# Kernel optimization log

Hardware: AMD Instinct MI355X
Metric: run time of the kernel (lower is better)

The kernel has to match this reference:

```python
import jax, jax.numpy as jnp
import numpy as np

B, H, W, D = 8, 56, 56, 256
NH = 8
KD = D // NH  # 32, key_dim == head_dim (value_factor=1)
FFN = 1024
EPS = 1e-6
SCALE = KD ** -0.5


def _lin(x, w, b):
    # torch nn.Linear: y = x @ W^T + b, W is (out, in)
    return jnp.einsum('...i,oi->...o', x, w) + b


def _ln(x, g, b):
    mu = jnp.mean(x, axis=-1, keepdims=True)
    var = jnp.mean(jnp.square(x - mu), axis=-1, keepdims=True)
    return (x - mu) * jax.lax.rsqrt(var + EPS) * g + b


def _dwconv(x, kernel, bias):
    # x: (B,H,W,C) NHWC, kernel: (kh,kw,1,C) HWIO depthwise
    y = jax.lax.conv_general_dilated(
        x, kernel, window_strides=(1, 1), padding='SAME',
        dimension_numbers=('NHWC', 'HWIO', 'NHWC'),
        feature_group_count=x.shape[-1])
    return y + bias


def _rope_sincos(h, w, head_dim):
    # PosEncodingGen: angle freq repeated pairwise, index over flattened H*W
    angle = 1.0 / (10000.0 ** jnp.linspace(0.0, 1.0, head_dim // 2))
    angle = jnp.repeat(angle, 2)  # (head_dim,)
    idx = jnp.arange(h * w, dtype=jnp.float32)
    phase = idx[:, None] * angle[None, :]
    return jnp.sin(phase).reshape(h, w, head_dim), jnp.cos(phase).reshape(h, w, head_dim)


def _angle_transform(x, sin, cos):
    # x: (B,NH,H,W,KD); sin/cos: (H,W,KD) broadcast over (B,NH)
    x1 = x[..., ::2]
    x2 = x[..., 1::2]
    rot = jnp.stack([-x2, x1], axis=-1).reshape(x.shape)
    return x * cos + rot * sin


def setup_inputs() -> dict:
    key = jax.random.key(0)
    ks = jax.random.split(key, 16)
    s = 0.02
    return {
        'x': jax.random.normal(ks[0], (B, H, W, D), jnp.float32),
        'cpe_w': jax.random.normal(ks[1], (3, 3, 1, D), jnp.float32) * s,
        'cpe_b': jnp.zeros((D,), jnp.float32),
        'ln1_g': jnp.ones((D,), jnp.float32),
        'ln1_b': jnp.zeros((D,), jnp.float32),
        'wq': jax.random.normal(ks[2], (D, D), jnp.float32) * s,
        'bq': jnp.zeros((D,), jnp.float32),
        'wk': jax.random.normal(ks[3], (D, D), jnp.float32) * s,
        'bk': jnp.zeros((D,), jnp.float32),
        'wv': jax.random.normal(ks[4], (D, D), jnp.float32) * s,
        'bv': jnp.zeros((D,), jnp.float32),
        'lepe_w': jax.random.normal(ks[5], (5, 5, 1, D), jnp.float32) * s,
        'lepe_b': jnp.zeros((D,), jnp.float32),
        'wo': jax.random.normal(ks[6], (D, D), jnp.float32) * s,
        'bo': jnp.zeros((D,), jnp.float32),
        'ln2_g': jnp.ones((D,), jnp.float32),
        'ln2_b': jnp.zeros((D,), jnp.float32),
        'fc1_w': jax.random.normal(ks[7], (FFN, D), jnp.float32) * s,
        'fc1_b': jnp.zeros((FFN,), jnp.float32),
        'dw_w': jax.random.normal(ks[8], (3, 3, 1, FFN), jnp.float32) * s,
        'dw_b': jnp.zeros((FFN,), jnp.float32),
        'fc2_w': jax.random.normal(ks[9], (D, FFN), jnp.float32) * s,
        'fc2_b': jnp.zeros((D,), jnp.float32),
    }


def _decomposed_gsa(x, sin, cos, wq, bq, wk, bk, wv, bv, lepe_w, lepe_b, wo, bo):
    b, h, w, d = x.shape
    q = _lin(x, wq, bq)
    k = _lin(x, wk, bk) * SCALE
    v = _lin(x, wv, bv)
    lepe = _dwconv(v, lepe_w, lepe_b)  # (b,h,w,d)
    # -> (b, nh, h, w, kd)
    q = q.reshape(b, h, w, NH, KD).transpose(0, 3, 1, 2, 4)
    k = k.reshape(b, h, w, NH, KD).transpose(0, 3, 1, 2, 4)
    v = v.reshape(b, h, w, NH, KD).transpose(0, 3, 1, 2, 4)
    qr = _angle_transform(q, sin, cos)
    kr = _angle_transform(k, sin, cos)
    # attention along W axis (per row h)
    aw = jnp.einsum('bnhik,bnhjk->bnhij', qr, kr)  # (b,nh,h,w,w)
    aw = jax.nn.softmax(aw, axis=-1)
    vw = jnp.einsum('bnhij,bnhjd->bnhid', aw, v)   # (b,nh,h,w,kd)
    # attention along H axis (per column w)
    ah = jnp.einsum('bniwk,bnjwk->bnwij', qr, kr)  # (b,nh,w,h,h)
    ah = jax.nn.softmax(ah, axis=-1)
    out = jnp.einsum('bnwij,bnjwd->bniwd', ah, vw)  # (b,nh,h,w,kd)
    # faithful to torch: flat reinterpret of (b,nh,h,w,kd) -> (b,h,w,nh*kd)
    out = out.reshape(b, h, w, NH * KD)
    out = out + lepe
    return _lin(out, wo, bo)


def reference(x, cpe_w, cpe_b, ln1_g, ln1_b, wq, bq, wk, bk, wv, bv,
              lepe_w, lepe_b, wo, bo, ln2_g, ln2_b,
              fc1_w, fc1_b, dw_w, dw_b, fc2_w, fc2_b):
    b, h, w, d = x.shape
    x = x + _dwconv(x, cpe_w, cpe_b)
    sin, cos = _rope_sincos(h, w, KD)
    # attention sub-block
    shortcut = x
    xn = _ln(x, ln1_g, ln1_b)
    attn = _decomposed_gsa(xn, sin, cos, wq, bq, wk, bk, wv, bv,
                           lepe_w, lepe_b, wo, bo)
    x = shortcut + attn  # drop_path=Identity, gamma_1=1.0
    # FFN sub-block (subconv=True, subln=False)
    shortcut = x
    xn = _ln(x, ln2_g, ln2_b)
    hdn = jax.nn.gelu(_lin(xn, fc1_w, fc1_b), approximate=False)
    hdn = _dwconv(hdn, dw_w, dw_b) + hdn
    ffn_out = _lin(hdn, fc2_w, fc2_b)
    return shortcut + ffn_out
```

## Files before the change

kernel.cpp:

```cpp
#include <hip/hip_runtime.h>
#include <hip/hip_bf16.h>
#include <math.h>

typedef __hip_bfloat16 bf16;

#define HB 8
#define HH 56
#define WWD 56
#define DD 256
#define NHEAD 8
#define KDIM 32
#define FFND 1024
#define NPIX (HB*HH*WWD)
#define SCALE_K 0.17677669529663687f

typedef __attribute__((ext_vector_type(8))) short short8;
typedef __attribute__((ext_vector_type(4))) float f32x4;

__device__ inline float toF(float x){ return x; }
__device__ inline float toF(bf16 x){ return __bfloat162float(x); }

__device__ inline float bfu_to_f(unsigned short u){
    union { float f; unsigned u32; } cv; cv.u32 = (unsigned)u << 16; return cv.f;
}

__device__ inline unsigned short f2bu(float f){
    union { bf16 b; unsigned short u; } cv; cv.b = __float2bfloat16(f); return cv.u;
}
__device__ inline unsigned pk2(float a, float b){
    return (unsigned)f2bu(a) | ((unsigned)f2bu(b) << 16);
}

__device__ inline void gl16(const bf16* g, unsigned short* l){
    __builtin_amdgcn_global_load_lds((const __attribute__((address_space(1))) void*)g,
                                     (__attribute__((address_space(3))) void*)l, 16, 0, 0);
}

__global__ __launch_bounds__(256) void wcvt_kernel(
    const float* __restrict__ wq, const float* __restrict__ wk,
    const float* __restrict__ wv, const float* __restrict__ wo,
    const float* __restrict__ f1, const float* __restrict__ f2,
    bf16* __restrict__ dst)
{
    const int id = blockIdx.x*256 + threadIdx.x;
    const float* src; int off;
    if      (id < 8192)  { src = wq; off = id; }
    else if (id < 16384) { src = wk; off = id - 8192; }
    else if (id < 24576) { src = wv; off = id - 16384; }
    else if (id < 32768) { src = wo; off = id - 24576; }
    else if (id < 65536) { src = f1; off = id - 32768; }
    else                 { src = f2; off = id - 65536; }
    const float4 a = *(const float4*)(src + (size_t)off*8);
    const float4 b = *(const float4*)(src + (size_t)off*8 + 4);
    uint4 v; v.x = pk2(a.x,a.y); v.y = pk2(a.z,a.w); v.z = pk2(b.x,b.y); v.w = pk2(b.z,b.w);
    *(uint4*)(dst + (size_t)id*8) = v;
}

__global__ __launch_bounds__(256) void rope_init_kernel(float2* __restrict__ t)
{
    const int id = blockIdx.x*256 + threadIdx.x;
    const int idx = id >> 4, i = id & 15;
    const float ph = (float)idx * exp2f(-(float)i * 0.88584749196996324f);
    t[id] = make_float2(cosf(ph), sinf(ph));
}

__global__ __launch_bounds__(256) void cpe_ln_kernel(
    const float* __restrict__ x, const float* __restrict__ wt,
    const float* __restrict__ bias, const float* __restrict__ g,
    const float* __restrict__ bln, float* __restrict__ X0, bf16* __restrict__ B1)
{
    constexpr int C = 256, VEC = 4, CG = 64, PPB = 4, KS = 3, P = 1;
    const int tid = threadIdx.x;
    const int cg  = tid % CG;
    const int pl  = tid / CG;
    const int p   = blockIdx.x * PPB + pl;
    const int w   = p % WWD;
    const int h   = (p / WWD) % HH;
    const int b   = p / (WWD * HH);
    const int c0  = cg * VEC;

    float acc[VEC];
    {
        const float4 b0 = *(const float4*)(bias + c0);
        acc[0] = b0.x; acc[1] = b0.y; acc[2] = b0.z; acc[3] = b0.w;
    }
    #pragma unroll
    for (int ky = 0; ky < KS; ky++) {
        const int hh = h + ky - P;
        if (hh < 0 || hh >= HH) continue;
        #pragma unroll
        for (int kx = 0; kx < KS; kx++) {
            const int ww = w + kx - P;
            if (ww < 0 || ww >= WWD) continue;
            const float4 wv = *(const float4*)(wt + (size_t)(ky*KS + kx)*C + c0);
            const float4 f0 = *(const float4*)(x + ((size_t)((b*HH + hh)*WWD + ww))*C + c0);
            acc[0] += f0.x * wv.x; acc[1] += f0.y * wv.y;
            acc[2] += f0.z * wv.z; acc[3] += f0.w * wv.w;
        }
    }
    const size_t obase = (size_t)p*C + c0;
    {
        const float4 f0 = *(const float4*)(x + obase);
        acc[0] += f0.x; acc[1] += f0.y; acc[2] += f0.z; acc[3] += f0.w;
    }
    { float4 o; o.x = acc[0]; o.y = acc[1]; o.z = acc[2]; o.w = acc[3];
      *(float4*)(X0 + obase) = o; }
    float s1 = acc[0] + acc[1] + acc[2] + acc[3];
    float s2 = acc[0]*acc[0] + acc[1]*acc[1] + acc[2]*acc[2] + acc[3]*acc[3];
    #pragma unroll
    for (int d = 1; d < 64; d <<= 1) { s1 += __shfl_xor(s1, d); s2 += __shfl_xor(s2, d); }
    const float mu  = s1 * (1.0f/DD);
    const float var = s2 * (1.0f/DD) - mu*mu;
    const float inv = rsqrtf(var + 1e-6f);
    const float4 gv = *(const float4*)(g + c0);
    const float4 bv = *(const float4*)(bln + c0);
    uint2 o;
    o.x = pk2((acc[0]-mu)*inv*gv.x + bv.x, (acc[1]-mu)*inv*gv.y + bv.y);
    o.y = pk2((acc[2]-mu)*inv*gv.z + bv.z, (acc[3]-mu)*inv*gv.w + bv.w);
    *(uint2*)(B1 + obase) = o;
}

template<int KS, bool ADD, int C>
__global__ __launch_bounds__(256) void dwconv_slide_kernel(
    const bf16* __restrict__ in, const float* __restrict__ wt, int wst,
    const float* __restrict__ bias, bf16* __restrict__ out)
{
    constexpr int VEC = 8, CG = C/VEC, GPB = 256/CG, NPX = 4, P = KS/2, NX = NPX+KS-1;
    constexpr int GPR = WWD/NPX;
    constexpr int NB  = NPIX/(NPX*GPB);
    const int tid = threadIdx.x;
    const int cg  = tid % CG;
    const int gl  = tid / CG;
    const int bid = blockIdx.x;
    const int swb = (bid & 7) * (NB >> 3) + (bid >> 3);
    const int gid = swb * GPB + gl;
    const int row = gid / GPR;
    const int w0  = (gid % GPR) * NPX;
    const int h   = row % HH;
    const int b   = row / HH;
    const int c0  = cg * VEC;

    float acc[NPX][VEC];
    {
        const float4 b0 = *(const float4*)(bias + c0);
        const float4 b1 = *(const float4*)(bias + c0 + 4);
        #pragma unroll
        for (int j = 0; j < NPX; j++) {
            acc[j][0]=b0.x; acc[j][1]=b0.y; acc[j][2]=b0.z; acc[j][3]=b0.w;
            acc[j][4]=b1.x; acc[j][5]=b1.y; acc[j][6]=b1.z; acc[j][7]=b1.w;
        }
    }

    #pragma unroll
    for (int ky = 0; ky < KS; ky++) {
        const int hh = h + ky - P;
        if (hh < 0 || hh >= HH) continue;
        const bf16* rowp = in + ((size_t)(b*HH + hh) * WWD) * C + c0;
        float wv[KS][VEC];
        #pragma unroll
        for (int kx = 0; kx < KS; kx++) {
            const float* wp = wt + (size_t)(ky*KS + kx)*wst + c0;
            const float4 w0v = *(const float4*)(wp);
            const float4 w1v = *(const float4*)(wp + 4);
            wv[kx][0]=w0v.x; wv[kx][1]=w0v.y; wv[kx][2]=w0v.z; wv[kx][3]=w0v.w;
            wv[kx][4]=w1v.x; wv[kx][5]=w1v.y; wv[kx][6]=w1v.z; wv[kx][7]=w1v.w;
        }
        #pragma unroll
        for (int x = 0; x < NX; x++) {
            const int ww = w0 - P + x;
            short8 raw = {0,0,0,0,0,0,0,0};
            if (ww >= 0 && ww < WWD) raw = *(const short8*)(rowp + (size_t)ww*C);
            float f[VEC];
            #pragma unroll
            for (int e = 0; e < VEC; e++) f[e] = bfu_to_f((unsigned short)raw[e]);
            #pragma unroll
            for (int j = 0; j < NPX; j++) {
                const int kx = x - j;
                if (kx < 0 || kx >= KS) continue;
                #pragma unroll
                for (int e = 0; e < VEC; e++)
                    acc[j][e] += f[e] * wv[kx][e];
            }
        }
    }

    #pragma unroll
    for (int j = 0; j < NPX; j++) {
        const size_t obase = ((size_t)row*WWD + w0 + j)*C + c0;
        if constexpr (ADD) {
            short8 vv = *(const short8*)(in + obase);
            #pragma unroll
            for (int e = 0; e < VEC; e++) acc[j][e] += bfu_to_f((unsigned short)vv[e]);
        }
        uint4 o;
        o.x = pk2(acc[j][0], acc[j][1]); o.y = pk2(acc[j][2], acc[j][3]);
        o.z = pk2(acc[j][4], acc[j][5]); o.w = pk2(acc[j][6], acc[j][7]);
        *(uint4*)(out + obase) = o;
    }
}

__global__ __launch_bounds__(256) void ln_kernel(
    const float* __restrict__ x, const float* __restrict__ g,
    const float* __restrict__ b, bf16* __restrict__ out)
{
    const int wv   = threadIdx.x >> 6;
    const int lane = threadIdx.x & 63;
    const int t    = blockIdx.x * 4 + wv;
    const float4 xv = *(const float4*)(x + (size_t)t*DD + lane*4);
    float s1 = xv.x + xv.y + xv.z + xv.w;
    float s2 = xv.x*xv.x + xv.y*xv.y + xv.z*xv.z + xv.w*xv.w;
    #pragma unroll
    for (int d = 1; d < 64; d <<= 1) {
        s1 += __shfl_xor(s1, d);
        s2 += __shfl_xor(s2, d);
    }
    const float mu  = s1 * (1.0f/DD);
    const float var = s2 * (1.0f/DD) - mu*mu;
    const float inv = rsqrtf(var + 1e-6f);
    const float4 gv = *(const float4*)(g + lane*4);
    const float4 bv = *(const float4*)(b + lane*4);
    uint2 o;
    o.x = pk2((xv.x-mu)*inv*gv.x + bv.x, (xv.y-mu)*inv*gv.y + bv.y);
    o.y = pk2((xv.z-mu)*inv*gv.z + bv.z, (xv.w-mu)*inv*gv.w + bv.w);
    *(uint2*)(out + (size_t)t*DD + lane*4) = o;
}

template<int EPI, int ROPE>
__global__ __launch_bounds__(256) void mgemm128_kernel(
    const bf16* __restrict__ A, const bf16* __restrict__ Wb, int ldw,
    const float* __restrict__ bias, const float2* __restrict__ ropet,
    const float* __restrict__ residF, float* __restrict__ accF,
    bf16* __restrict__ outB, bf16* __restrict__ outK, bf16* __restrict__ outV,
    int M, int N, int K, float scale)
{
    __shared__ __align__(16) unsigned short Sh[8704];
    unsigned short* As = Sh;
    unsigned short* Bs = Sh + 4096;
    const int tid  = threadIdx.x;
    const int wid  = tid >> 6;
    const int lane = tid & 63;
    const int quad = lane >> 4;
    const int l15  = lane & 15;
    const int wr   = wid >> 1;
    const int wc   = wid & 1;

    const int NXg = gridDim.x;
    const int T   = NXg * gridDim.y;
    int f = blockIdx.y * NXg + blockIdx.x;
    f = (f & 7) * (T >> 3) + (f >> 3);
    const int row0 = (f / NXg) * 128;
    const int col0 = (f % NXg) * 128;

    f32x4 acc[4][4];
    #pragma unroll
    for (int m = 0; m < 4; m++)
        #pragma unroll
        for (int n = 0; n < 4; n++)
            acc[m][n] = (f32x4){0.f, 0.f, 0.f, 0.f};

    for (int k0 = 0; k0 < K; k0 += 32) {
        __syncthreads();
        #pragma unroll
        for (int j = 0; j < 2; j++) {
            const int ob  = (wid*2 + j)*64;
            const int o   = ob + lane;
            const int row = o >> 2;
            const int ch  = (o & 3) * 8;
            gl16(A  + (size_t)(row0 + row)*K   + k0 + ch, &As[ob*8]);
            gl16(Wb + (size_t)(col0 + row)*ldw + k0 + ch, &Bs[ob*8]);
        }
        __syncthreads();
        short8 af[4], bfr[4];
        #pragma unroll
        for (int m = 0; m < 4; m++)
            af[m] = *(const short8*)(&As[(wr*64 + m*16 + l15)*32 + quad*8]);
        #pragma unroll
        for (int n = 0; n < 4; n++)
            bfr[n] = *(const short8*)(&Bs[(wc*64 + n*16 + l15)*32 + quad*8]);
        #pragma unroll
        for (int m = 0; m < 4; m++)
            #pragma unroll
            for (int n = 0; n < 4; n++)
                acc[m][n] = __builtin_amdgcn_mfma_f32_16x16x32_bf16(af[m], bfr[n], acc[m][n], 0, 0, 0);
    }

    __syncthreads();
    float* Ls = (float*)Sh;
    const int cbl = l15 * 4;
    const int seg = (EPI == 3) ? (col0 >> 8) : 0;
    bf16* dst = outB;
    if (EPI == 3) dst = (seg == 0) ? outB : ((seg == 1) ? outK : outV);
    const float esc = (EPI == 3) ? ((seg == 1) ? scale : 1.0f) : scale;
    const bool doRope = ROPE && (EPI != 3 || seg < 2);

    #pragma unroll
    for (int m = 0; m < 4; m++) {
        #pragma unroll
        for (int n = 0; n < 4; n++) {
            const int col = n*16 + l15;
            const float bval = bias[col0 + wc*64 + col];
            #pragma unroll
            for (int reg = 0; reg < 4; reg++) {
                float y = (acc[m][n][reg] + bval) * esc;
                if (EPI == 1) y = 0.5f*y*(1.0f + erff(y*0.70710678118654752f));
                Ls[wid*1088 + (quad*4+reg)*68 + col] = y;
            }
        }
        #pragma unroll
        for (int p = 0; p < 4; p++) {
            const int rowt = p*4 + quad;
            const float4 v = *(const float4*)&Ls[wid*1088 + rowt*68 + cbl];
            const int mm = row0 + wr*64 + m*16 + rowt;
            if (EPI == 2) {
                const size_t o = (size_t)mm * N + col0 + wc*64 + cbl;
                const float4 rv = *(const float4*)(residF + o);
                float4 w; w.x = v.x+rv.x; w.y = v.y+rv.y; w.z = v.z+rv.z; w.w = v.w+rv.w;
                *(float4*)(accF + o) = w;
            } else {
                const int ncl = (EPI == 3) ? ((col0 & 255) + wc*64 + cbl)
                                           : (col0 + wc*64 + cbl);
                const size_t o = (EPI == 3) ? ((size_t)mm * 256 + ncl)
                                            : ((size_t)mm * N + ncl);
                float a = v.x, b = v.y, c = v.z, d = v.w;
                if (doRope) {
                    const int idx = mm % (HH*WWD);
                    const int i0 = (ncl & 31) >> 1;
                    const float4 t = *(const float4*)&ropet[(size_t)idx*16 + i0];
                    const float na  = a*t.x - b*t.y;
                    const float nb  = b*t.x + a*t.y;
                    const float ncv = c*t.z - d*t.w;
                    const float nd  = d*t.z + c*t.w;
                    a = na; b = nb; c = ncv; d = nd;
                }
                uint2 ov; ov.x = pk2(a, b); ov.y = pk2(c, d);
                *(uint2*)(dst + o) = ov;
            }
        }
    }
}

template<bool COLM>
__global__ __launch_bounds__(256) void attn_mfma_kernel(
    const bf16* __restrict__ q, const bf16* __restrict__ k,
    const bf16* __restrict__ v, const bf16* __restrict__ lepe,
    bf16* __restrict__ outp)
{
    __shared__ unsigned short Qb[64*40];
    __shared__ unsigned short Kb[64*40];
    __shared__ unsigned short Vt[32*80];
    __shared__ unsigned short Pb[64*72];

    const int bid  = blockIdx.x;
    const int line = bid % 56;
    const int nh   = (bid / 56) % NHEAD;
    const int b    = bid / (56 * NHEAD);
    const int tid  = threadIdx.x;
    const int wid  = tid >> 6;
    const int lane = tid & 63;
    const int quad = lane >> 4;
    const int l15  = lane & 15;

    const size_t rstr = COLM ? (size_t)WWD * DD : (size_t)DD;
    const size_t base = COLM ? (((size_t)b*HH*WWD + line) * DD + nh*KDIM)
                             : (((size_t)(b*HH + line) * WWD) * DD + nh*KDIM);

    {
        const int r  = tid >> 2;
        const int cc = tid & 3;
        uint4 zero = {0,0,0,0};
        if (r < 56) {
            size_t g = base + (size_t)r * rstr + cc*8;
            *(uint4*)(&Qb[r*40 + cc*8]) = *(const uint4*)(q + g);
            *(uint4*)(&Kb[r*40 + cc*8]) = *(const uint4*)(k + g);
        } else {
            *(uint4*)(&Qb[r*40 + cc*8]) = zero;
            *(uint4*)(&Kb[r*40 + cc*8]) = zero;
        }
        uint4 vv = zero;
        if (lane < 56)
            vv = *(const uint4*)(v + base + (size_t)lane * rstr + wid*8);
        const unsigned short* pv = (const unsigned short*)&vv;
        #pragma unroll
        for (int e = 0; e < 8; e++)
            Vt[(wid*8 + e)*80 + lane] = pv[e];
    }
    __syncthreads();

    {
        short8 af = *(const short8*)(&Qb[(wid*16 + l15)*40 + quad*8]);
        f32x4 s_[4];
        #pragma unroll
        for (int j = 0; j < 4; j++) {
            short8 bfm = *(const short8*)(&Kb[(j*16 + l15)*40 + quad*8]);
            f32x4 z = {0.f,0.f,0.f,0.f};
            s_[j] = __builtin_amdgcn_mfma_f32_16x16x32_bf16(af, bfm, z, 0, 0, 0);
        }
        const bool v3 = (l15 < 8);
        float mx[4], sm[4];
        #pragma unroll
        for (int reg = 0; reg < 4; reg++) {
            float m01 = fmaxf(s_[0][reg], s_[1][reg]);
            float m23 = v3 ? fmaxf(s_[2][reg], s_[3][reg]) : s_[2][reg];
            mx[reg] = fmaxf(m01, m23);
        }
        #pragma unroll
        for (int d = 1; d < 16; d <<= 1) {
            #pragma unroll
            for (int reg = 0; reg < 4; reg++)
                mx[reg] = fmaxf(mx[reg], __shfl_xor(mx[reg], d));
        }
        float e_[4][4];
        #pragma unroll
        for (int reg = 0; reg < 4; reg++) sm[reg] = 0.f;
        #pragma unroll
        for (int j = 0; j < 4; j++) {
            #pragma unroll
            for (int reg = 0; reg < 4; reg++) {
                const bool valid = (j < 3) || v3;
                float ex = valid ? expf(s_[j][reg] - mx[reg]) : 0.f;
                e_[j][reg] = ex;
                sm[reg] += ex;
            }
        }
        #pragma unroll
        for (int d = 1; d < 16; d <<= 1) {
            #pragma unroll
            for (int reg = 0; reg < 4; reg++)
                sm[reg] += __shfl_xor(sm[reg], d);
        }
        float inv[4];
        #pragma unroll
        for (int reg = 0; reg < 4; reg++) inv[reg] = 1.0f / sm[reg];
        #pragma unroll
        for (int j = 0; j < 4; j++)
            #pragma unroll
            for (int reg = 0; reg < 4; reg++)
                Pb[(wid*16 + quad*4 + reg)*72 + j*16 + l15] = f2bu(e_[j][reg] * inv[reg]);
    }
    __syncthreads();

    {
        f32x4 acc[2];
        acc[0] = (f32x4){0.f,0.f,0.f,0.f};
        acc[1] = (f32x4){0.f,0.f,0.f,0.f};
        #pragma unroll
        for (int k0 = 0; k0 < 64; k0 += 32) {
            short8 af = *(const short8*)(&Pb[(wid*16 + l15)*72 + k0 + quad*8]);
            #pragma unroll
            for (int nt = 0; nt < 2; nt++) {
                short8 bfm = *(const short8*)(&Vt[(nt*16 + l15)*80 + k0 + quad*8]);
                acc[nt] = __builtin_amdgcn_mfma_f32_16x16x32_bf16(af, bfm, acc[nt], 0, 0, 0);
            }
        }
        #pragma unroll
        for (int nt = 0; nt < 2; nt++) {
            #pragma unroll
            for (int reg = 0; reg < 4; reg++) {
                const int m = wid*16 + quad*4 + reg;
                const int d = nt*16 + l15;
                if (m < 56) {
                    float val = acc[nt][reg];
                    if (COLM) {
                        int hp = 7*nh + (m >> 3);
                        int wp = (m & 7)*7 + (line >> 3);
                        int cp = (line & 7)*32 + d;
                        size_t o = ((size_t)(b*HH + hp)*WWD + wp)*DD + cp;
                        outp[o] = __float2bfloat16(val + toF(lepe[o]));
                    } else {
                        outp[base + (size_t)m * rstr + d] = __float2bfloat16(val);
                    }
                }
            }
        }
    }
}

extern "C" void kernel_launch(void* const* d_in, const int* in_sizes, int n_in,
                              void* d_out, int out_size, void* d_ws, size_t ws_size,
                              hipStream_t stream)
{
    const float* x_in   = (const float*)d_in[0];
    const float* cpe_w  = (const float*)d_in[1];
    const float* cpe_b  = (const float*)d_in[2];
    const float* ln1_g  = (const float*)d_in[3];
    const float* ln1_b  = (const float*)d_in[4];
    const float* wq     = (const float*)d_in[5];
    const float* bq     = (const float*)d_in[6];
    const float* wk     = (const float*)d_in[7];
    const float* bk     = (const float*)d_in[8];
    const float* wv     = (const float*)d_in[9];
    const float* bv     = (const float*)d_in[10];
    const float* lepe_w = (const float*)d_in[11];
    const float* lepe_b = (const float*)d_in[12];
    const float* wo     = (const float*)d_in[13];
    const float* bo     = (const float*)d_in[14];
    const float* ln2_g  = (const float*)d_in[15];
    const float* ln2_b  = (const float*)d_in[16];
    const float* fc1_w  = (const float*)d_in[17];
    const float* fc1_b  = (const float*)d_in[18];
    const float* dw_w   = (const float*)d_in[19];
    const float* dw_b   = (const float*)d_in[20];
    const float* fc2_w  = (const float*)d_in[21];
    const float* fc2_b  = (const float*)d_in[22];
    float* out = (float*)d_out;

    const size_t ND = (size_t)NPIX * DD;
    const size_t NF = (size_t)NPIX * FFND;
    char* ws = (char*)d_ws;
    float*  X0    = (float*)(ws);
    float*  ACC   = (float*)(ws + ND*4);
    bf16*   B1    = (bf16*) (ws + ND*8);
    bf16*   B2    = (bf16*) (ws + ND*8 + ND*2);
    bf16*   H1    = (bf16*) (ws + ND*8 + ND*4);
    bf16*   H2    = (bf16*) (ws + ND*8 + ND*4 + NF*2);
    bf16*   WB    = (bf16*) (ws + ND*8 + ND*4 + NF*4);
    float2* ROPET = (float2*)(ws + ND*8 + ND*4 + NF*4 + 786432*2);
    float*  BQKV  = (float*) (ws + ND*8 + ND*4 + NF*4 + 786432*2 + 50176*8);
    bf16*   B3 = H1;
    bf16*   B4 = H2;
    bf16*   VWb   = (bf16*)d_out;
    bf16*   ATTNb = VWb + ND;

    const bf16* WOb = WB + 196608;
    const bf16* F1b = WB + 262144;
    const bf16* F2b = WB + 524288;

    dim3 b256(256);
    dim3 gridQKV(768/128, NPIX/128);
    dim3 gridD(DD/128, NPIX/128);
    dim3 gridF(FFND/128, NPIX/128);

    wcvt_kernel<<<384, b256, 0, stream>>>(wq, wk, wv, wo, fc1_w, fc2_w, WB);
    rope_init_kernel<<<196, b256, 0, stream>>>(ROPET);
    hipMemcpyAsync(BQKV,       bq, 256*sizeof(float), hipMemcpyDeviceToDevice, stream);
    hipMemcpyAsync(BQKV + 256, bk, 256*sizeof(float), hipMemcpyDeviceToDevice, stream);
    hipMemcpyAsync(BQKV + 512, bv, 256*sizeof(float), hipMemcpyDeviceToDevice, stream);
    cpe_ln_kernel<<<NPIX/4, b256, 0, stream>>>(x_in, cpe_w, cpe_b, ln1_g, ln1_b, X0, B1);
    mgemm128_kernel<3,1><<<gridQKV, b256, 0, stream>>>(B1, WB, DD, BQKV, ROPET,
                                                       nullptr, nullptr, B2, B3, B4,
                                                       NPIX, 768, DD, SCALE_K);
    dwconv_slide_kernel<5, false, 256><<<784, b256, 0, stream>>>(B4, lepe_w, DD, lepe_b, B1);
    attn_mfma_kernel<false><<<HB*NHEAD*HH, b256, 0, stream>>>(B2, B3, B4, nullptr, VWb);
    attn_mfma_kernel<true><<<HB*NHEAD*WWD, b256, 0, stream>>>(B2, B3, VWb, B1, ATTNb);
    mgemm128_kernel<2,0><<<gridD, b256, 0, stream>>>(ATTNb, WOb, DD, bo, nullptr,
                                                     X0, ACC, nullptr, nullptr, nullptr,
                                                     NPIX, DD, DD, 1.0f);
    ln_kernel<<<NPIX/4, b256, 0, stream>>>(ACC, ln2_g, ln2_b, B2);
    mgemm128_kernel<1,0><<<gridF, b256, 0, stream>>>(B2, F1b, DD, fc1_b, nullptr,
                                                     nullptr, nullptr, H1, nullptr, nullptr,
                                                     NPIX, FFND, DD, 1.0f);
    dwconv_slide_kernel<3, true, 1024><<<3136, b256, 0, stream>>>(H1, dw_w, FFND, dw_b, H2);
    mgemm128_kernel<2,0><<<gridD, b256, 0, stream>>>(H2, F2b, FFND, fc2_b, nullptr,
                                                     ACC, out, nullptr, nullptr, nullptr,
                                                     NPIX, DD, FFND, 1.0f);
}
```

Before: 347.7 us.

## Double-buffer LDS tiles in MFMA GEMM to overlap global loads with compute

Converts the GEMM main loop to a two-stage LDS ping-pong: the next K-slice is issued via direct-to-LDS loads while MFMAs run on the current buffer, synchronised with explicit vmcnt waits and barriers. Address pointers are precomputed and incremented instead of being recomputed each iteration. LDS use doubles to 32KB per block, which may reduce occupancy. The epilogue gains extra barriers per m-iteration because it reuses the shared buffer.

```diff
diff --git a/kernel.cpp b/kernel.cpp
--- a/kernel.cpp
+++ b/kernel.cpp
@@ -233,9 +233,7 @@
     bf16* __restrict__ outB, bf16* __restrict__ outK, bf16* __restrict__ outV,
     int M, int N, int K, float scale)
 {
-    __shared__ __align__(16) unsigned short Sh[8704];
-    unsigned short* As = Sh;
-    unsigned short* Bs = Sh + 4096;
+    __shared__ __align__(16) unsigned short Sh[16384];
     const int tid  = threadIdx.x;
     const int wid  = tid >> 6;
     const int lane = tid & 63;
@@ -258,31 +256,53 @@
         for (int n = 0; n < 4; n++)
             acc[m][n] = (f32x4){0.f, 0.f, 0.f, 0.f};
 
-    for (int k0 = 0; k0 < K; k0 += 32) {
-        __syncthreads();
-        #pragma unroll
-        for (int j = 0; j < 2; j++) {
-            const int ob  = (wid*2 + j)*64;
-            const int o   = ob + lane;
-            const int row = o >> 2;
-            const int ch  = (o & 3) * 8;
-            gl16(A  + (size_t)(row0 + row)*K   + k0 + ch, &As[ob*8]);
-            gl16(Wb + (size_t)(col0 + row)*ldw + k0 + ch, &Bs[ob*8]);
-        }
-        __syncthreads();
-        short8 af[4], bfr[4];
-        #pragma unroll
-        for (int m = 0; m < 4; m++)
-            af[m] = *(const short8*)(&As[(wr*64 + m*16 + l15)*32 + quad*8]);
-        #pragma unroll
-        for (int n = 0; n < 4; n++)
-            bfr[n] = *(const short8*)(&Bs[(wc*64 + n*16 + l15)*32 + quad*8]);
-        #pragma unroll
-        for (int m = 0; m < 4; m++)
-            #pragma unroll
-            for (int n = 0; n < 4; n++)
-                acc[m][n] = __builtin_amdgcn_mfma_f32_16x16x32_bf16(af[m], bfr[n], acc[m][n], 0, 0, 0);
-    }
+    const int ob0 = (wid*2 + 0)*64;
+    const int ob1 = (wid*2 + 1)*64;
+    const int o0  = ob0 + lane, o1 = ob1 + lane;
+    const int rA0 = o0 >> 2, ch0 = (o0 & 3)*8;
+    const int rA1 = o1 >> 2, ch1 = (o1 & 3)*8;
+    const bf16* pA0 = A  + (size_t)(row0 + rA0)*K   + ch0;
+    const bf16* pA1 = A  + (size_t)(row0 + rA1)*K   + ch1;
+    const bf16* pW0 = Wb + (size_t)(col0 + rA0)*ldw + ch0;
+    const bf16* pW1 = Wb + (size_t)(col0 + rA1)*ldw + ch1;
+
+    #define STAGE(bi) { unsigned short* As_ = Sh + (bi)*8192;                  \
+                        unsigned short* Bs_ = Sh + (bi)*8192 + 4096;           \
+                        gl16(pA0, &As_[ob0*8]); gl16(pA1, &As_[ob1*8]);        \
+                        gl16(pW0, &Bs_[ob0*8]); gl16(pW1, &Bs_[ob1*8]);        \
+                        pA0 += 32; pA1 += 32; pW0 += 32; pW1 += 32; }
+
+    #define COMPUTE(bi) { const unsigned short* As_ = Sh + (bi)*8192;          \
+                          const unsigned short* Bs_ = Sh + (bi)*8192 + 4096;   \
+                          short8 af[4], bfr[4];                                \
+                          _Pragma("unroll")                                    \
+                          for (int m = 0; m < 4; m++)                          \
+                              af[m] = *(const short8*)(&As_[(wr*64 + m*16 + l15)*32 + quad*8]); \
+                          _Pragma("unroll")                                    \
+                          for (int n = 0; n < 4; n++)                          \
+                              bfr[n] = *(const short8*)(&Bs_[(wc*64 + n*16 + l15)*32 + quad*8]); \
+                          _Pragma("unroll")                                    \
+                          for (int m = 0; m < 4; m++)                          \
+                              _Pragma("unroll")                                \
+                              for (int n = 0; n < 4; n++)                      \
+                                  acc[m][n] = __builtin_amdgcn_mfma_f32_16x16x32_bf16(af[m], bfr[n], acc[m][n], 0, 0, 0); }
+
+    const int nt = K >> 5;
+    STAGE(0);
+    int cur = 0;
+    for (int t = 0; t < nt - 1; t++) {
+        STAGE(cur ^ 1);
+        asm volatile("s_waitcnt vmcnt(4)" ::: "memory");
+        __builtin_amdgcn_s_barrier();
+        COMPUTE(cur);
+        __builtin_amdgcn_s_barrier();
+        cur ^= 1;
+    }
+    asm volatile("s_waitcnt vmcnt(0)" ::: "memory");
+    __builtin_amdgcn_s_barrier();
+    COMPUTE(cur);
+    #undef STAGE
+    #undef COMPUTE
 
     __syncthreads();
     float* Ls = (float*)Sh;
@@ -336,6 +356,7 @@
                 *(uint2*)(dst + o) = ov;
             }
         }
+        if (m < 3) __syncthreads();
     }
 }
 
```

New measurement: 330.5 us. -4.9%, faster.
